# Kernel optimization log

Hardware: AMD Instinct MI355X
Metric: run time of the kernel (lower is better)

## Reference

```python
import jax, jax.numpy as jnp
import numpy as np

TWO_PI = 2.0 * np.pi


def setup_inputs() -> dict:
    key = jax.random.key(0)
    k1, k2, k3, k4 = jax.random.split(key, 4)
    N, H, W, B = 1024, 256, 256, 64
    pred = jax.random.uniform(k1, (N,), dtype=jnp.float32)
    mu = jax.random.uniform(k2, (N, 2), dtype=jnp.float32)              # centers in [0,1]
    sigma = jax.random.uniform(k3, (N, 2), dtype=jnp.float32) * 0.25 + 0.05  # widths in [0.05,0.30]
    nodes = jnp.concatenate([mu, sigma], axis=1)                         # [N,4]
    batch_list = jax.random.randint(k4, (N,), 0, B, dtype=jnp.int64)
    return {"pred": pred, "nodes": nodes, "batch_list": batch_list,
            "h": H, "w": W, "batch_num": B}


def reference(pred, nodes, batch_list, h, w, batch_num):
    # Normalized grid, identical to torch.arange(num)*step + start
    xs = jnp.linspace(0.0, 1.0, w, dtype=pred.dtype)   # [w]
    ys = jnp.linspace(0.0, 1.0, h, dtype=pred.dtype)   # [h]
    x_t = xs[None, :]                                   # broadcasts to [h,w]
    y_t = ys[:, None]

    mu_x = nodes[:, 0][:, None, None]
    mu_y = nodes[:, 1][:, None, None]
    sx = nodes[:, 2][:, None, None]
    sy = nodes[:, 3][:, None, None]

    # [N,h,w] per-node gaussian (epsilon = 0 in the original module)
    g = (1.0 / (TWO_PI * sx * sy)) * jnp.exp(
        -((x_t[None] - mu_x) ** 2 / (2.0 * sx ** 2)
          + (y_t[None] - mu_y) ** 2 / (2.0 * sy ** 2)))

    # normalize each node map by its max, scale by pred[i]
    g = g / jnp.max(g, axis=(1, 2), keepdims=True) * pred[:, None, None]

    # scatter-add into per-batch maps
    maps = jax.ops.segment_sum(g, batch_list, num_segments=batch_num)   # [B,h,w]
    return maps[:, None, :, :]                                          # [B,1,h,w]
```

## Files before the change

### kernel.cpp

```cpp
#include <hip/hip_runtime.h>
#include <math.h>

#define HCONST 256
#define WCONST 256
#define TILE_Y 32

__global__ __launch_bounds__(512) void prep_kernel(
    const float* __restrict__ pred,
    const float* __restrict__ nodes,
    float* __restrict__ Fx,
    float* __restrict__ Fy)
{
    const int n = blockIdx.x;
    const int t = threadIdx.x;
    const bool isY = (t >= WCONST);
    const int  i   = t & (WCONST - 1);

    const float4 nd = ((const float4*)nodes)[n];
    const float mu = isY ? nd.y : nd.x;
    const float s  = isY ? nd.w : nd.z;
    const float a  = 1.0f / (2.0f * s * s);

    const float step = 1.0f / 255.0f;
    const float d = i * step - mu;

    float ni = roundf(mu * 255.0f);
    ni = fminf(fmaxf(ni, 0.0f), 255.0f);
    const float dmin = ni * step - mu;

    float val = __expf(-a * (d * d - dmin * dmin));
    if (isY) val *= pred[n];

    (isY ? Fy : Fx)[n * WCONST + i] = val;
}

__global__ __launch_bounds__(1024) void bucket_kernel(
    const int* __restrict__ batch_list, int N, int B,
    int* __restrict__ offsets, int* __restrict__ indices)
{
    __shared__ int cnt[64];
    __shared__ int base[65];
    const int t = threadIdx.x;

    if (t < B) cnt[t] = 0;
    __syncthreads();

    for (int n = t; n < N; n += blockDim.x)
        atomicAdd(&cnt[batch_list[n]], 1);
    __syncthreads();

    if (t == 0) {
        int acc = 0;
        for (int b = 0; b < B; ++b) { base[b] = acc; acc += cnt[b]; }
        base[B] = acc;
    }
    __syncthreads();

    if (t <= B) offsets[t] = base[t];
    if (t < B)  cnt[t] = base[t];
    __syncthreads();

    for (int n = t; n < N; n += blockDim.x) {
        const int b   = batch_list[n];
        const int pos = atomicAdd(&cnt[b], 1);
        indices[pos] = n;
    }
}

__global__ __launch_bounds__(256) void accum_kernel(
    const float* __restrict__ Fx, const float* __restrict__ Fy,
    const int* __restrict__ offsets, const int* __restrict__ indices,
    float* __restrict__ out)
{
    const int tiles = HCONST / TILE_Y;
    const int b  = blockIdx.x / tiles;
    const int ty = blockIdx.x % tiles;
    const int y0 = ty * TILE_Y;
    const int x  = threadIdx.x;

    float acc[TILE_Y];
#pragma unroll
    for (int yy = 0; yy < TILE_Y; ++yy) acc[yy] = 0.0f;

    const int g0 = offsets[b];
    const int g1 = offsets[b + 1];
    for (int g = g0; g < g1; ++g) {
        const int n = indices[g];
        const float fxv = Fx[n * WCONST + x];
        const float* fy = &Fy[n * HCONST + y0];
#pragma unroll
        for (int yy = 0; yy < TILE_Y; ++yy)
            acc[yy] = fmaf(fy[yy], fxv, acc[yy]);
    }

    float* o = out + ((size_t)b * HCONST + y0) * WCONST + x;
#pragma unroll
    for (int yy = 0; yy < TILE_Y; ++yy)
        o[yy * WCONST] = acc[yy];
}

extern "C" void kernel_launch(void* const* d_in, const int* in_sizes, int n_in,
                              void* d_out, int out_size, void* d_ws, size_t ws_size,
                              hipStream_t stream) {
    const float* pred       = (const float*)d_in[0];
    const float* nodes      = (const float*)d_in[1];
    const int*   batch_list = (const int*)d_in[2];

    const int N = in_sizes[0];
    const int B = out_size / (HCONST * WCONST);

    float* out = (float*)d_out;

    float* Fx = (float*)d_ws;
    float* Fy = Fx + (size_t)N * WCONST;
    int* offsets = (int*)(Fy + (size_t)N * HCONST);
    int* indices = offsets + (B + 1);

    prep_kernel<<<N, 512, 0, stream>>>(pred, nodes, Fx, Fy);
    bucket_kernel<<<1, 1024, 0, stream>>>(batch_list, N, B, offsets, indices);
    accum_kernel<<<B * (HCONST / TILE_Y), 256, 0, stream>>>(Fx, Fy, offsets, indices, out);
}
```

Measured before the change: 81.62 us.

## Fuse prep, bucketing and accumulation into a single kernel with on-the-fly gaussians

```diff
diff --git a/kernel.cpp b/kernel.cpp
--- a/kernel.cpp
+++ b/kernel.cpp
@@ -3,94 +3,65 @@
 
 #define HCONST 256
 #define WCONST 256
-#define TILE_Y 32
+#define NMAX   1024
+#define TILE_Y 16
+#define TILES  (HCONST / TILE_Y)
 
-__global__ __launch_bounds__(512) void prep_kernel(
+__global__ __launch_bounds__(WCONST) void fused_kernel(
     const float* __restrict__ pred,
     const float* __restrict__ nodes,
-    float* __restrict__ Fx,
-    float* __restrict__ Fy)
+    const int*   __restrict__ batch_list,
+    int N,
+    float* __restrict__ out)
 {
-    const int n = blockIdx.x;
-    const int t = threadIdx.x;
-    const bool isY = (t >= WCONST);
-    const int  i   = t & (WCONST - 1);
+    const int b  = blockIdx.x / TILES;
+    const int ty = blockIdx.x % TILES;
+    const int y0 = ty * TILE_Y;
+    const int x  = threadIdx.x;
 
-    const float4 nd = ((const float4*)nodes)[n];
-    const float mu = isY ? nd.y : nd.x;
-    const float s  = isY ? nd.w : nd.z;
-    const float a  = 1.0f / (2.0f * s * s);
-
-    const float step = 1.0f / 255.0f;
-    const float d = i * step - mu;
-
-    float ni = roundf(mu * 255.0f);
-    ni = fminf(fmaxf(ni, 0.0f), 255.0f);
-    const float dmin = ni * step - mu;
-
-    float val = __expf(-a * (d * d - dmin * dmin));
-    if (isY) val *= pred[n];
-
-    (isY ? Fy : Fx)[n * WCONST + i] = val;
-}
-
-__global__ __launch_bounds__(1024) void bucket_kernel(
-    const int* __restrict__ batch_list, int N, int B,
-    int* __restrict__ offsets, int* __restrict__ indices)
-{
-    __shared__ int cnt[64];
-    __shared__ int base[65];
-    const int t = threadIdx.x;
-
-    if (t < B) cnt[t] = 0;
+    __shared__ int s_idx[NMAX];
+    __shared__ int s_cnt;
+    if (x == 0) s_cnt = 0;
     __syncthreads();
-
-    for (int n = t; n < N; n += blockDim.x)
-        atomicAdd(&cnt[batch_list[n]], 1);
-    __syncthreads();
-
-    if (t == 0) {
-        int acc = 0;
-        for (int b = 0; b < B; ++b) { base[b] = acc; acc += cnt[b]; }
-        base[B] = acc;
+    for (int n = x; n < N; n += WCONST) {
+        if (batch_list[n] == b) {
+            int p = atomicAdd(&s_cnt, 1);
+            s_idx[p] = n;
+        }
     }
     __syncthreads();
-
-    if (t <= B) offsets[t] = base[t];
-    if (t < B)  cnt[t] = base[t];
-    __syncthreads();
-
-    for (int n = t; n < N; n += blockDim.x) {
-        const int b   = batch_list[n];
-        const int pos = atomicAdd(&cnt[b], 1);
-        indices[pos] = n;
-    }
-}
-
-__global__ __launch_bounds__(256) void accum_kernel(
-    const float* __restrict__ Fx, const float* __restrict__ Fy,
-    const int* __restrict__ offsets, const int* __restrict__ indices,
-    float* __restrict__ out)
-{
-    const int tiles = HCONST / TILE_Y;
-    const int b  = blockIdx.x / tiles;
-    const int ty = blockIdx.x % tiles;
-    const int y0 = ty * TILE_Y;
-    const int x  = threadIdx.x;
+    const int cnt = s_cnt;
 
     float acc[TILE_Y];
 #pragma unroll
     for (int yy = 0; yy < TILE_Y; ++yy) acc[yy] = 0.0f;
 
-    const int g0 = offsets[b];
-    const int g1 = offsets[b + 1];
-    for (int g = g0; g < g1; ++g) {
-        const int n = indices[g];
-        const float fxv = Fx[n * WCONST + x];
-        const float* fy = &Fy[n * HCONST + y0];
+    const float step  = 1.0f / 255.0f;
+    const float xs    = x * step;
+    const float ylane = (y0 + (x & (TILE_Y - 1))) * step;
+
+    for (int g = 0; g < cnt; ++g) {
+        const int n = s_idx[g];
+        const float4 nd = ((const float4*)nodes)[n];
+        const float pr = pred[n];
+
+        const float ax = 1.0f / (2.0f * nd.z * nd.z);
+        const float ay = 1.0f / (2.0f * nd.w * nd.w);
+
+        const float nix = fminf(fmaxf(roundf(nd.x * 255.0f), 0.0f), 255.0f);
+        const float niy = fminf(fmaxf(roundf(nd.y * 255.0f), 0.0f), 255.0f);
+        const float dxm = nix * step - nd.x;
+        const float dym = niy * step - nd.y;
+
+        const float dx = xs - nd.x;
+        const float fx = __expf(-ax * (dx * dx - dxm * dxm)) * pr;
+
+        const float dy  = ylane - nd.y;
+        const float fyv = __expf(-ay * (dy * dy - dym * dym));
+
 #pragma unroll
         for (int yy = 0; yy < TILE_Y; ++yy)
-            acc[yy] = fmaf(fy[yy], fxv, acc[yy]);
+            acc[yy] = fmaf(__shfl(fyv, yy, TILE_Y), fx, acc[yy]);
     }
 
     float* o = out + ((size_t)b * HCONST + y0) * WCONST + x;
@@ -111,12 +82,5 @@
 
     float* out = (float*)d_out;
 
-    float* Fx = (float*)d_ws;
-    float* Fy = Fx + (size_t)N * WCONST;
-    int* offsets = (int*)(Fy + (size_t)N * HCONST);
-    int* indices = offsets + (B + 1);
-
-    prep_kernel<<<N, 512, 0, stream>>>(pred, nodes, Fx, Fy);
-    bucket_kernel<<<1, 1024, 0, stream>>>(batch_list, N, B, offsets, indices);
-    accum_kernel<<<B * (HCONST / TILE_Y), 256, 0, stream>>>(Fx, Fy, offsets, indices, out);
+    fused_kernel<<<B * TILES, WCONST, 0, stream>>>(pred, nodes, batch_list, N, out);
 }
```

After: 87.35 us. 1.07x slower.
